# Kernel tuning notes

Hardware: AMD Instinct MI355X
Metric: run time of the kernel (lower is better)

Reference implementation:

```python
import jax, jax.numpy as jnp
import numpy as np

B, T, O, H = 64, 1000, 61, 256
IN0, IN1 = 320, 2 * H  # layer0 input = 8*40 flattened feats; layer1 input = bidirectional concat


def setup_inputs() -> dict:
    key = jax.random.key(0)
    ks = jax.random.split(key, 12)
    rn = lambda k, shape: (jax.random.normal(k, shape, dtype=jnp.float32) * 0.05)
    inp = {}
    inp["batch"] = jax.random.normal(ks[0], (B, T, 8, 40), dtype=jnp.float32)
    lengths = np.random.RandomState(0).randint(T // 2, T + 1, size=B).astype(np.int64)
    inp["lengths"] = jnp.asarray(lengths)
    # GRU params stacked over directions: [2, 3H, in], [2, 3H, H], biases [2, 3H]
    inp["w_ih_l0"] = rn(ks[1], (2, 3 * H, IN0))
    inp["w_hh_l0"] = rn(ks[2], (2, 3 * H, H))
    inp["b_ih_l0"] = rn(ks[3], (2, 3 * H))
    inp["b_hh_l0"] = rn(ks[4], (2, 3 * H))
    inp["w_ih_l1"] = rn(ks[5], (2, 3 * H, IN1))
    inp["w_hh_l1"] = rn(ks[6], (2, 3 * H, H))
    inp["b_ih_l1"] = rn(ks[7], (2, 3 * H))
    inp["b_hh_l1"] = rn(ks[8], (2, 3 * H))
    inp["fc_w"] = rn(ks[9], (O, 2 * H))
    inp["fc_b"] = rn(ks[10], (O,))
    return inp


def _gru_dir(x, w_ih, w_hh, b_ih, b_hh, reverse):
    # x: [T, B, in] -> ys: [T, B, H]; torch GRU cell semantics
    def step(h, xt):
        gi = xt @ w_ih.T + b_ih          # [B, 3H]
        gh = h @ w_hh.T + b_hh           # [B, 3H]
        i_r, i_z, i_n = jnp.split(gi, 3, axis=-1)
        h_r, h_z, h_n = jnp.split(gh, 3, axis=-1)
        r = jax.nn.sigmoid(i_r + h_r)
        z = jax.nn.sigmoid(i_z + h_z)
        n = jnp.tanh(i_n + r * h_n)
        h_new = (1.0 - z) * n + z * h
        return h_new, h_new
    h0 = jnp.zeros((x.shape[1], w_hh.shape[-1]), x.dtype)
    _, ys = jax.lax.scan(step, h0, x, reverse=reverse)
    return ys


def _bigru_layer(x, w_ih, w_hh, b_ih, b_hh):
    fwd = _gru_dir(x, w_ih[0], w_hh[0], b_ih[0], b_hh[0], reverse=False)
    bwd = _gru_dir(x, w_ih[1], w_hh[1], b_ih[1], b_hh[1], reverse=True)
    return jnp.concatenate([fwd, bwd], axis=-1)  # [T, B, 2H]


def reference(batch, lengths, w_ih_l0, w_hh_l0, b_ih_l0, b_hh_l0,
              w_ih_l1, w_hh_l1, b_ih_l1, b_hh_l1, fc_w, fc_b):
    b, t = batch.shape[0], batch.shape[1]
    x = jnp.swapaxes(batch, 2, 3).reshape(b, t, -1)   # transpose(2,3).flatten(2) -> [B,T,320]
    x = jnp.swapaxes(x, 0, 1)                          # [T, B, 320] (time-major like torch GRU)
    h1 = _bigru_layer(x, w_ih_l0, w_hh_l0, b_ih_l0, b_hh_l0)
    h2 = _bigru_layer(h1, w_ih_l1, w_hh_l1, b_ih_l1, b_hh_l1)
    out = h2 @ fc_w.T + fc_b                           # [T, B, O]
    out = jnp.swapaxes(out, 0, 1)                      # [B, T, O]
    # gather first lengths[i] timesteps of each sample, concatenated
    L = np.asarray(lengths)
    mask = np.arange(t)[None, :] < L[:, None]
    bi, ti = np.nonzero(mask)
    return out[bi, ti]                                 # [sum(lengths), O]
```

## Files before the change

kernel.cpp:

```cpp
#include <hip/hip_runtime.h>
#include <cstdint>
#include <cstddef>


typedef __attribute__((ext_vector_type(8))) __bf16 bf16x8;
typedef __attribute__((ext_vector_type(4))) float f32x4;
typedef __attribute__((ext_vector_type(4))) unsigned int u32x4;

#define AS1 __attribute__((address_space(1)))
#define AS3 __attribute__((address_space(3)))

#define LOG2E 1.44269504089f
#define SRZ  (-1.44269504089f)
#define SN   (2.88539008177f)

__device__ __forceinline__ void async_ld16(const void* g, void* l) {
  __builtin_amdgcn_global_load_lds((const AS1 unsigned int*)g,
                                   (AS3 unsigned int*)l, 16, 0, 0);
}

__device__ __forceinline__ f32x4 mfma16(u32x4 a, u32x4 b, f32x4 c) {
  return __builtin_amdgcn_mfma_f32_16x16x32_bf16(
      __builtin_bit_cast(bf16x8, a), __builtin_bit_cast(bf16x8, b), c, 0, 0, 0);
}

__device__ __forceinline__ unsigned short f2b(float f) {
  unsigned int u = __float_as_uint(f);
  u += 0x7fffu + ((u >> 16) & 1u);
  return (unsigned short)(u >> 16);
}
__device__ __forceinline__ float b2f(unsigned short s) {
  return __uint_as_float(((unsigned int)s) << 16);
}
__device__ __forceinline__ float gload(const float* p, size_t i) { return p[i]; }
__device__ __forceinline__ float gload(const unsigned short* p, size_t i) { return b2f(p[i]); }
__device__ __forceinline__ void gstore(float* p, size_t i, float v) { p[i] = v; }
__device__ __forceinline__ void gstore(unsigned short* p, size_t i, float v) { p[i] = f2b(v); }

__device__ __forceinline__ float sigm2(float xs) {
  return __builtin_amdgcn_rcpf(1.0f + __builtin_amdgcn_exp2f(xs));
}
__device__ __forceinline__ float tanh2(float ys) {
  return __builtin_fmaf(-2.0f,
      __builtin_amdgcn_rcpf(1.0f + __builtin_amdgcn_exp2f(ys)), 1.0f);
}

__device__ __forceinline__ void lds_barrier() {
  asm volatile("" ::: "memory");
  __builtin_amdgcn_s_waitcnt(0xC07F);
  __builtin_amdgcn_s_barrier();
  asm volatile("" ::: "memory");
}

__global__ void cast_bf16_kernel(const float* __restrict__ src,
                                 unsigned short* __restrict__ dst, int n) {
  const int i = blockIdx.x * 256 + threadIdx.x;
  if (i < n) dst[i] = f2b(src[i]);
}

__global__ void cast_w_kernel(const float* __restrict__ src,
                              unsigned short* __restrict__ dst, int n,
                              int in_dim) {
  const int i = blockIdx.x * 256 + threadIdx.x;
  if (i < n) {
    const int row = (i / in_dim) % 768;
    const float s = (row < 512) ? SRZ : SN;
    dst[i] = f2b(s * src[i]);
  }
}

__global__ void bias_fuse_kernel(const float* __restrict__ bih,
                                 const float* __restrict__ bhh,
                                 float* __restrict__ fb) {
  const int n = blockIdx.x * 256 + threadIdx.x;
  if (n < 1536) {
    const int dir = n >> 9 >> 1 ? 1 : (n / 768);
    const int rr = n - dir * 768;
    const float s = (rr < 512) ? SRZ : SN;
    float v = bih[dir * 768 + rr];
    if (rr < 512) v += bhh[dir * 768 + rr];
    fb[n] = s * v;
  }
}

__global__ void transpose_x_kernel(const float* __restrict__ batch,
                                   unsigned short* __restrict__ xb) {
  const int t = blockIdx.x, b = blockIdx.y, i = threadIdx.x;
  const float v = batch[((size_t)b * 1000 + t) * 320 + (i & 7) * 40 + (i >> 3)];
  xb[((size_t)t * 64 + b) * 320 + i] = f2b(v);
}

template <typename CT>
__global__ __launch_bounds__(256) void gemm_bt_kernel(
    const unsigned short* __restrict__ A, const unsigned short* __restrict__ W,
    const float* __restrict__ bias, CT* __restrict__ C, int M, int N, int K) {
  __shared__ __align__(16) unsigned short As[4096];
  __shared__ __align__(16) unsigned short Bs[4096];
  const int tid = threadIdx.x;
  const int lane = tid & 63;
  const int wv = tid >> 6;
  const int mBase = blockIdx.x * 128;
  const int nBase = blockIdx.y * 128;

  const int s0 = tid, s1 = tid + 256;
  const int r0 = ((s0 >> 6) << 4) | (s0 & 15), c0 = ((s0 >> 4) & 3) * 8;
  const int r1 = ((s1 >> 6) << 4) | (s1 & 15), c1 = ((s1 >> 4) & 3) * 8;

  const unsigned short* Arow0 = A + (size_t)(mBase + r0) * K + c0;
  const unsigned short* Arow1 = A + (size_t)(mBase + r1) * K + c1;
  const unsigned short* Wrow0 = W + (size_t)(nBase + r0) * K + c0;
  const unsigned short* Wrow1 = W + (size_t)(nBase + r1) * K + c1;

  char* lA = (char*)As;
  char* lB = (char*)Bs;
  char* dstA0 = lA + wv * 1024;
  char* dstA1 = lA + 4096 + wv * 1024;
  char* dstB0 = lB + wv * 1024;
  char* dstB1 = lB + 4096 + wv * 1024;

  f32x4 acc[4][4] = {};
  const int mh = (wv >> 1) * 64, nh = (wv & 1) * 64;
  const u32x4* As4 = (const u32x4*)As;
  const u32x4* Bs4 = (const u32x4*)Bs;

  for (int k0 = 0; k0 < K; k0 += 32) {
    __syncthreads();
    async_ld16(Arow0 + k0, dstA0);
    async_ld16(Arow1 + k0, dstA1);
    async_ld16(Wrow0 + k0, dstB0);
    async_ld16(Wrow1 + k0, dstB1);
    __syncthreads();
    u32x4 a[4], b[4];
#pragma unroll
    for (int mt = 0; mt < 4; ++mt) a[mt] = As4[((mh >> 4) + mt) * 64 + lane];
#pragma unroll
    for (int nt = 0; nt < 4; ++nt) b[nt] = Bs4[((nh >> 4) + nt) * 64 + lane];
#pragma unroll
    for (int mt = 0; mt < 4; ++mt)
#pragma unroll
      for (int nt = 0; nt < 4; ++nt)
        acc[mt][nt] = mfma16(a[mt], b[nt], acc[mt][nt]);
  }
#pragma unroll
  for (int nt = 0; nt < 4; ++nt) {
    const int n = nBase + nh + nt * 16 + (lane & 15);
    const float bn = bias[n];
#pragma unroll
    for (int mt = 0; mt < 4; ++mt) {
      const int mrow = mBase + mh + mt * 16 + ((lane >> 4) << 2);
#pragma unroll
      for (int r = 0; r < 4; ++r)
        gstore(C, (size_t)(mrow + r) * N + n, acc[mt][nt][r] + bn);
    }
  }
}

template <typename GT>
__global__ __launch_bounds__(512, 2) void gru_fast_kernel(
    const GT* __restrict__ gi,
    const unsigned short* __restrict__ whh,
    const float* __restrict__ bhh,
    unsigned short* __restrict__ hout) {
  constexpr int E = (int)sizeof(GT);
  constexpr int CH = (E * 1536) / 1024;
  extern __shared__ __align__(16) char smem[];
  char* wlds = smem;
  char* hl   = smem + 98304;
  char* glds = smem + 98304 + 9216;
  const int tid = threadIdx.x;
  const int lane = tid & 63;
  const int w = tid >> 6;
  const int c = lane & 15;
  const int q = lane >> 4;
  const int dir = blockIdx.x & 1;
  const int sb = (blockIdx.x >> 1) * 16;

  for (int i = tid; i < 4608; i += 512) ((unsigned short*)hl)[i] = 0;

  const int u0 = 32 * w + c;
  const float bhn0 = SN * bhh[dir * 768 + 512 + u0];
  const float bhn1 = SN * bhh[dir * 768 + 512 + u0 + 16];

  const unsigned short* wb =
      whh + (size_t)dir * 196608 + (size_t)u0 * 256 + q * 8;
  u32x4 wv[2][3][6];
#pragma unroll
  for (int j = 0; j < 2; ++j)
#pragma unroll
    for (int g = 0; g < 3; ++g) {
      const unsigned short* p = wb + (size_t)(g * 256 + 16 * j) * 256;
#pragma unroll
      for (int kt = 0; kt < 6; ++kt) wv[j][g][kt] = *(const u32x4*)(p + kt * 32);
#pragma unroll
      for (int kk = 0; kk < 2; ++kk) {
        u32x4 tmp = *(const u32x4*)(p + (6 + kk) * 32);
        *(u32x4*)(wlds + (((w * 12 + (j * 3 + g) * 2 + kk) << 10) + lane * 16)) = tmp;
      }
    }
#pragma unroll
  for (int j = 0; j < 2; ++j)
#pragma unroll
    for (int g = 0; g < 3; ++g)
#pragma unroll
      for (int kt = 0; kt < 6; ++kt)
        asm volatile("" : "+v"(wv[j][g][kt]));

  float h0[4] = {0.f, 0.f, 0.f, 0.f}, h1[4] = {0.f, 0.f, 0.f, 0.f};

  const int t0 = dir ? 999 : 0;
  unsigned short* hp = hout + ((size_t)t0 * 64 + sb) * 512 + dir * 256 + u0;
  const ptrdiff_t gstep = (dir ? -1 : 1) * (ptrdiff_t)(64 * 1536);
  const ptrdiff_t hstep = (dir ? -1 : 1) * (ptrdiff_t)(64 * 512);

  char* gdw = glds + w * (1536 * E);
  const int off0 = (c ^ ((q & 1) << 4)) * E;
  const int off1 = ((c + 16) ^ ((q & 1) << 4)) * E;
  const char* grb0 = gdw + (q * 4) * (96 * E) + off0;
  const char* grb1 = gdw + (q * 4) * (96 * E) + off1;
  const GT* gs[CH];
#pragma unroll
  for (int i = 0; i < CH; ++i) {
    const int p    = i * 64 + lane;
    const int s    = p / (6 * E);
    const int rem  = p - s * (6 * E);
    const int g    = rem / (2 * E);
    const int subp = rem - g * (2 * E);
    const int sub  = subp ^ (((s >> 2) & 1) * E);
    const int col  = sub * (16 / E);
    gs[i] = gi + ((size_t)t0 * 64 + sb + s) * 1536 + dir * 768 + 32 * w +
            g * 256 + col;
  }
#pragma unroll
  for (int i = 0; i < CH; ++i) {
    async_ld16(gs[i], gdw + i * 1024);
    gs[i] += gstep;
  }

  __syncthreads();

  const char* habase = hl + c * 576 + q * 16;
  const int hw0 = q * 4 * 288 + u0;

  for (int step = 0; step < 1000; ++step) {
    u32x4 a[8];
#pragma unroll
    for (int kt = 0; kt < 8; ++kt) a[kt] = *(const u32x4*)(habase + kt * 64);
    lds_barrier();

    f32x4 acc[2][3] = {};
#pragma unroll
    for (int kt = 0; kt < 6; ++kt)
#pragma unroll
      for (int j = 0; j < 2; ++j)
#pragma unroll
        for (int g = 0; g < 3; ++g)
          acc[j][g] = mfma16(a[kt], wv[j][g][kt], acc[j][g]);
#pragma unroll
    for (int kk = 0; kk < 2; ++kk) {
      u32x4 bf[2][3];
#pragma unroll
      for (int j = 0; j < 2; ++j)
#pragma unroll
        for (int g = 0; g < 3; ++g)
          bf[j][g] = *(const u32x4*)(
              wlds + (((w * 12 + (j * 3 + g) * 2 + kk) << 10) + lane * 16));
#pragma unroll
      for (int j = 0; j < 2; ++j)
#pragma unroll
        for (int g = 0; g < 3; ++g)
          acc[j][g] = mfma16(a[6 + kk], bf[j][g], acc[j][g]);
    }

    asm volatile("s_waitcnt vmcnt(0)" ::: "memory");
    float pv0[3][4], pv1[3][4];
#pragma unroll
    for (int r = 0; r < 4; ++r)
#pragma unroll
      for (int g = 0; g < 3; ++g) {
        pv0[g][r] = gload((const GT*)(grb0 + (r * 96 + g * 32) * E), (size_t)0);
        pv1[g][r] = gload((const GT*)(grb1 + (r * 96 + g * 32) * E), (size_t)0);
      }

    unsigned short* hls = (unsigned short*)hl;
#pragma unroll
    for (int r = 0; r < 4; ++r) {
      const float rr0 = sigm2(pv0[0][r] + acc[0][0][r]);
      const float zz0 = sigm2(pv0[1][r] + acc[0][1][r]);
      const float nn0 = tanh2(__builtin_fmaf(rr0, acc[0][2][r] + bhn0, pv0[2][r]));
      const float hv0 = __builtin_fmaf(zz0, h0[r] - nn0, nn0);
      h0[r] = hv0;
      const float rr1 = sigm2(pv1[0][r] + acc[1][0][r]);
      const float zz1 = sigm2(pv1[1][r] + acc[1][1][r]);
      const float nn1 = tanh2(__builtin_fmaf(rr1, acc[1][2][r] + bhn1, pv1[2][r]));
      const float hv1 = __builtin_fmaf(zz1, h1[r] - nn1, nn1);
      h1[r] = hv1;
      const unsigned short hb0 = f2b(hv0), hb1 = f2b(hv1);
      hls[hw0 + r * 288] = hb0;
      hls[hw0 + r * 288 + 16] = hb1;
      hp[(size_t)(q * 4 + r) * 512] = hb0;
      hp[(size_t)(q * 4 + r) * 512 + 16] = hb1;
    }

#pragma unroll
    for (int i = 0; i < CH; ++i) {
      async_ld16(gs[i], gdw + i * 1024);
      gs[i] += gstep;
    }
    hp += hstep;
    lds_barrier();
  }
}

template <typename GT>
__global__ __launch_bounds__(1024) void gru_layer_kernel(
    const GT* __restrict__ gi, const unsigned short* __restrict__ whh,
    const float* __restrict__ bhh, unsigned short* __restrict__ hout) {
  __shared__ __align__(16) unsigned short hbf[16][264];
  __shared__ __align__(16) float gh[16][780];
  const int tid = threadIdx.x;
  const int lane = tid & 63;
  const int wv = tid >> 6;
  const int dir = blockIdx.x & 1;
  const int sb = (blockIdx.x >> 1) * 16;
  const int j = tid & 255;
  const int si = tid >> 8;

  float hreg[4] = {0.f, 0.f, 0.f, 0.f};
#pragma unroll
  for (int i = 0; i < 4; ++i) hbf[si + i * 4][j] = 0;

  const float bh_n = SN * bhh[dir * 768 + 512 + j];

  const unsigned short* wl = whh + (size_t)dir * 768 * 256 +
                             (size_t)(wv * 48 + (lane & 15)) * 256 +
                             ((lane >> 4) * 8);
  const char* habase = (const char*)hbf + (lane & 15) * 528 + ((lane >> 4) << 4);
  const int srow = (lane >> 4) * 4;

  __syncthreads();

  for (int step = 0; step < 1000; ++step) {
    const int t = dir ? (999 - step) : step;
    float p_ir[4], p_iz[4], p_in[4];
#pragma unroll
    for (int i = 0; i < 4; ++i) {
      const int s = si + i * 4;
      const size_t gib = ((size_t)t * 64 + (sb + s)) * 1536 + dir * 768 + j;
      p_ir[i] = gload(gi, gib);
      p_iz[i] = gload(gi, gib + 256);
      p_in[i] = gload(gi, gib + 512);
    }
    u32x4 a[8];
#pragma unroll
    for (int kt = 0; kt < 8; ++kt) a[kt] = *(const u32x4*)(habase + kt * 64);
#pragma unroll
    for (int ntd = 0; ntd < 3; ++ntd) {
      f32x4 acc = {0.f, 0.f, 0.f, 0.f};
#pragma unroll
      for (int kt = 0; kt < 8; ++kt) {
        u32x4 bfrag = *(const u32x4*)(wl + ntd * (16 * 256) + kt * 32);
        acc = mfma16(a[kt], bfrag, acc);
      }
      const int gcol = (wv * 3 + ntd) * 16 + (lane & 15);
#pragma unroll
      for (int r = 0; r < 4; ++r) gh[srow + r][gcol] = acc[r];
    }
    __syncthreads();
#pragma unroll
    for (int i = 0; i < 4; ++i) {
      const int s = si + i * 4;
      const float r = sigm2(p_ir[i] + gh[s][j]);
      const float z = sigm2(p_iz[i] + gh[s][256 + j]);
      const float n = tanh2(__builtin_fmaf(r, gh[s][512 + j] + bh_n, p_in[i]));
      const float h = __builtin_fmaf(z, hreg[i] - n, n);
      hreg[i] = h;
      const unsigned short hb = f2b(h);
      hbf[s][j] = hb;
      hout[((size_t)t * 64 + (sb + s)) * 512 + dir * 256 + j] = hb;
    }
    __syncthreads();
  }
}

__global__ void prefix_kernel(const int* __restrict__ raw,
                              int* __restrict__ pref, int* __restrict__ lens) {
  if (threadIdx.x == 0) {
    const int stride = (raw[1] == 0 && raw[3] == 0 && raw[5] == 0) ? 2 : 1;
    int a = 0;
    for (int b = 0; b < 64; ++b) {
      const int L = raw[b * stride];
      pref[b] = a;
      lens[b] = L;
      a += L;
    }
  }
}

__global__ __launch_bounds__(256) void fc_kernel(
    const unsigned short* __restrict__ h2, const unsigned short* __restrict__ fcw,
    const float* __restrict__ fcb, const int* __restrict__ lens,
    const int* __restrict__ pref, float* __restrict__ out) {
  __shared__ __align__(16) unsigned short hrow[4][512];
  const int b = blockIdx.y;
  const int sub = threadIdx.x >> 6, lane = threadIdx.x & 63;
  const int t = blockIdx.x * 4 + sub;
  *(u32x4*)&hrow[sub][lane * 8] =
      *(const u32x4*)&h2[((size_t)t * 64 + b) * 512 + lane * 8];
  __syncthreads();
  const int len = lens[b];
  if (lane < 61 && t < len) {
    float acc = fcb[lane];
    const unsigned short* wr = fcw + (size_t)lane * 512;
#pragma unroll 4
    for (int k = 0; k < 512; k += 8) {
      u32x4 w4 = *(const u32x4*)(wr + k);
      u32x4 h4 = *(const u32x4*)(&hrow[sub][k]);
#pragma unroll
      for (int qq = 0; qq < 4; ++qq) {
        acc += __uint_as_float(w4[qq] << 16) * __uint_as_float(h4[qq] << 16);
        acc += __uint_as_float(w4[qq] & 0xffff0000u) * __uint_as_float(h4[qq] & 0xffff0000u);
      }
    }
    out[((size_t)pref[b] + t) * 61 + lane] = acc;
  }
}

template <typename GT>
static void run_pipeline(const float* batch, const int* lengths_raw,
                         const float* w_ih_l0, const float* w_hh_l0,
                         const float* b_ih_l0, const float* b_hh_l0,
                         const float* w_ih_l1, const float* w_hh_l1,
                         const float* b_ih_l1, const float* b_hh_l1,
                         const float* fc_w, const float* fc_b, float* out,
                         char* ws, hipStream_t stream) {
  size_t off = 0;
  auto alloc = [&](size_t bytes) -> char* {
    char* p = ws + off;
    off += (bytes + 255) & ~(size_t)255;
    return p;
  };
  char* pool = alloc((size_t)64000 * 512 * 2);
  unsigned short* xb = (unsigned short*)pool;
  unsigned short* h1 = (unsigned short*)pool;
  unsigned short* h2 = (unsigned short*)pool;
  GT*             gi   = (GT*)alloc((size_t)64064 * 1536 * sizeof(GT));
  unsigned short* wih0 = (unsigned short*)alloc((size_t)1536 * 320 * 2);
  unsigned short* wih1 = (unsigned short*)alloc((size_t)1536 * 512 * 2);
  unsigned short* whh0 = (unsigned short*)alloc((size_t)1536 * 256 * 2);
  unsigned short* whh1 = (unsigned short*)alloc((size_t)1536 * 256 * 2);
  unsigned short* fcwb = (unsigned short*)alloc((size_t)61 * 512 * 2);
  float*          fb0  = (float*)alloc(1536 * 4);
  float*          fb1  = (float*)alloc(1536 * 4);
  int*            pref = (int*)alloc(256);
  int*            lens = (int*)alloc(256);

  auto castw = [&](const float* s, unsigned short* d, int n, int in_dim) {
    cast_w_kernel<<<dim3((n + 255) / 256), dim3(256), 0, stream>>>(s, d, n, in_dim);
  };
  castw(w_ih_l0, wih0, 2 * 768 * 320, 320);
  castw(w_hh_l0, whh0, 2 * 768 * 256, 256);
  castw(w_ih_l1, wih1, 2 * 768 * 512, 512);
  castw(w_hh_l1, whh1, 2 * 768 * 256, 256);
  cast_bf16_kernel<<<dim3((61 * 512 + 255) / 256), dim3(256), 0, stream>>>(
      fc_w, fcwb, 61 * 512);
  bias_fuse_kernel<<<dim3(6), dim3(256), 0, stream>>>(b_ih_l0, b_hh_l0, fb0);
  bias_fuse_kernel<<<dim3(6), dim3(256), 0, stream>>>(b_ih_l1, b_hh_l1, fb1);

  transpose_x_kernel<<<dim3(1000, 64), dim3(320), 0, stream>>>(batch, xb);

  const int GRU_LDS = 98304 + 9216 + 8 * 1536 * (int)sizeof(GT);
  const bool big_lds =
      hipFuncSetAttribute(reinterpret_cast<const void*>(gru_fast_kernel<GT>),
                          hipFuncAttributeMaxDynamicSharedMemorySize,
                          GRU_LDS) == hipSuccess;

  auto gru = [&](GT* g, unsigned short* w, const float* b, unsigned short* h) {
    if (big_lds)
      gru_fast_kernel<GT><<<dim3(8), dim3(512), GRU_LDS, stream>>>(g, w, b, h);
    else
      gru_layer_kernel<GT><<<dim3(8), dim3(1024), 0, stream>>>(g, w, b, h);
  };

  gemm_bt_kernel<GT><<<dim3(500, 12), dim3(256), 0, stream>>>(
      xb, wih0, fb0, gi, 64000, 1536, 320);
  gru(gi, whh0, b_hh_l0, h1);
  gemm_bt_kernel<GT><<<dim3(500, 12), dim3(256), 0, stream>>>(
      h1, wih1, fb1, gi, 64000, 1536, 512);
  gru(gi, whh1, b_hh_l1, h2);

  prefix_kernel<<<dim3(1), dim3(64), 0, stream>>>(lengths_raw, pref, lens);
  fc_kernel<<<dim3(250, 64), dim3(256), 0, stream>>>(h2, fcwb, fc_b, lens, pref, out);
}

extern "C" void kernel_launch(void* const* d_in, const int* in_sizes, int n_in,
                              void* d_out, int out_size, void* d_ws, size_t ws_size,
                              hipStream_t stream) {
  (void)in_sizes; (void)n_in; (void)out_size;
  const float* batch   = (const float*)d_in[0];
  const int*   lengths = (const int*)d_in[1];
  const float* w_ih_l0 = (const float*)d_in[2];
  const float* w_hh_l0 = (const float*)d_in[3];
  const float* b_ih_l0 = (const float*)d_in[4];
  const float* b_hh_l0 = (const float*)d_in[5];
  const float* w_ih_l1 = (const float*)d_in[6];
  const float* w_hh_l1 = (const float*)d_in[7];
  const float* b_ih_l1 = (const float*)d_in[8];
  const float* b_hh_l1 = (const float*)d_in[9];
  const float* fc_w    = (const float*)d_in[10];
  const float* fc_b    = (const float*)d_in[11];
  float* out = (float*)d_out;
  char* ws = (char*)d_ws;

  const size_t NEED_FP32 = 470000000ull;
  if (ws_size >= NEED_FP32) {
    run_pipeline<float>(batch, lengths, w_ih_l0, w_hh_l0, b_ih_l0, b_hh_l0,
                        w_ih_l1, w_hh_l1, b_ih_l1, b_hh_l1, fc_w, fc_b, out,
                        ws, stream);
  } else {
    run_pipeline<unsigned short>(batch, lengths, w_ih_l0, w_hh_l0, b_ih_l0,
                                 b_hh_l0, w_ih_l1, w_hh_l1, b_ih_l1, b_hh_l1,
                                 fc_w, fc_b, out, ws, stream);
  }
}
```

Measured before the change: 4.536 ms.

## Double-buffer GRU hidden state and interleave gate MFMAs with activations

For the bf16 gate-input path, the hidden-state LDS buffer is double-buffered so each step reads one copy and writes the other. This removes the barrier that sat between the h read and the matmul. The recurrent matmul is split per gate (r, then n, then z) so the sigmoid and tanh work on earlier gates can overlap the MFMAs of later ones. The async prefetch of the next step's gate inputs is issued earlier in the step. The cost is extra LDS per block and more live registers, and it relies on a single end-of-step barrier being enough for correctness.

```diff
diff --git a/kernel.cpp b/kernel.cpp
--- a/kernel.cpp
+++ b/kernel.cpp
@@ -155,6 +155,22 @@
   }
 }
 
+#define GBLOCK(G)                                                              \
+  {                                                                            \
+    _Pragma("unroll") for (int kt = 0; kt < 6; ++kt) {                         \
+      acc[0][G] = mfma16(a[kt], wv[0][G][kt], acc[0][G]);                      \
+      acc[1][G] = mfma16(a[kt], wv[1][G][kt], acc[1][G]);                      \
+    }                                                                          \
+    _Pragma("unroll") for (int kk = 0; kk < 2; ++kk) {                         \
+      u32x4 bf0 = *(const u32x4*)(wlds +                                       \
+          (((w * 12 + (0 * 3 + (G)) * 2 + kk) << 10) + lane * 16));            \
+      u32x4 bf1 = *(const u32x4*)(wlds +                                       \
+          (((w * 12 + (1 * 3 + (G)) * 2 + kk) << 10) + lane * 16));            \
+      acc[0][G] = mfma16(a[6 + kk], bf0, acc[0][G]);                           \
+      acc[1][G] = mfma16(a[6 + kk], bf1, acc[1][G]);                           \
+    }                                                                          \
+  }
+
 template <typename GT>
 __global__ __launch_bounds__(512, 2) void gru_fast_kernel(
     const GT* __restrict__ gi,
@@ -163,10 +179,12 @@
     unsigned short* __restrict__ hout) {
   constexpr int E = (int)sizeof(GT);
   constexpr int CH = (E * 1536) / 1024;
+  constexpr bool DB = (E == 2);
+  constexpr int HB = DB ? 18432 : 9216;
   extern __shared__ __align__(16) char smem[];
   char* wlds = smem;
   char* hl   = smem + 98304;
-  char* glds = smem + 98304 + 9216;
+  char* glds = smem + 98304 + HB;
   const int tid = threadIdx.x;
   const int lane = tid & 63;
   const int w = tid >> 6;
@@ -175,7 +193,7 @@
   const int dir = blockIdx.x & 1;
   const int sb = (blockIdx.x >> 1) * 16;
 
-  for (int i = tid; i < 4608; i += 512) ((unsigned short*)hl)[i] = 0;
+  for (int i = tid; i < HB / 2; i += 512) ((unsigned short*)hl)[i] = 0;
 
   const int u0 = 32 * w + c;
   const float bhn0 = SN * bhh[dir * 768 + 512 + u0];
@@ -241,35 +259,15 @@
   const char* habase = hl + c * 576 + q * 16;
   const int hw0 = q * 4 * 288 + u0;
 
-  for (int step = 0; step < 1000; ++step) {
+  auto body = [&](int rd, int wr) {
     u32x4 a[8];
 #pragma unroll
-    for (int kt = 0; kt < 8; ++kt) a[kt] = *(const u32x4*)(habase + kt * 64);
-    lds_barrier();
+    for (int kt = 0; kt < 8; ++kt)
+      a[kt] = *(const u32x4*)(habase + rd + kt * 64);
+    if constexpr (!DB) lds_barrier();
 
     f32x4 acc[2][3] = {};
-#pragma unroll
-    for (int kt = 0; kt < 6; ++kt)
-#pragma unroll
-      for (int j = 0; j < 2; ++j)
-#pragma unroll
-        for (int g = 0; g < 3; ++g)
-          acc[j][g] = mfma16(a[kt], wv[j][g][kt], acc[j][g]);
-#pragma unroll
-    for (int kk = 0; kk < 2; ++kk) {
-      u32x4 bf[2][3];
-#pragma unroll
-      for (int j = 0; j < 2; ++j)
-#pragma unroll
-        for (int g = 0; g < 3; ++g)
-          bf[j][g] = *(const u32x4*)(
-              wlds + (((w * 12 + (j * 3 + g) * 2 + kk) << 10) + lane * 16));
-#pragma unroll
-      for (int j = 0; j < 2; ++j)
-#pragma unroll
-        for (int g = 0; g < 3; ++g)
-          acc[j][g] = mfma16(a[6 + kk], bf[j][g], acc[j][g]);
-    }
+    GBLOCK(0)
 
     asm volatile("s_waitcnt vmcnt(0)" ::: "memory");
     float pv0[3][4], pv1[3][4];
@@ -280,19 +278,39 @@
         pv0[g][r] = gload((const GT*)(grb0 + (r * 96 + g * 32) * E), (size_t)0);
         pv1[g][r] = gload((const GT*)(grb1 + (r * 96 + g * 32) * E), (size_t)0);
       }
-
-    unsigned short* hls = (unsigned short*)hl;
+    asm volatile("s_waitcnt lgkmcnt(0)" ::: "memory");
+#pragma unroll
+    for (int i = 0; i < CH; ++i) {
+      async_ld16(gs[i], gdw + i * 1024);
+      gs[i] += gstep;
+    }
+
+    float rr0[4], rr1[4];
 #pragma unroll
     for (int r = 0; r < 4; ++r) {
-      const float rr0 = sigm2(pv0[0][r] + acc[0][0][r]);
+      rr0[r] = sigm2(pv0[0][r] + acc[0][0][r]);
+      rr1[r] = sigm2(pv1[0][r] + acc[1][0][r]);
+    }
+
+    GBLOCK(2)
+
+    float nn0[4], nn1[4];
+#pragma unroll
+    for (int r = 0; r < 4; ++r) {
+      nn0[r] = tanh2(__builtin_fmaf(rr0[r], acc[0][2][r] + bhn0, pv0[2][r]));
+      nn1[r] = tanh2(__builtin_fmaf(rr1[r], acc[1][2][r] + bhn1, pv1[2][r]));
+    }
+
+    GBLOCK(1)
+
+    unsigned short* hls = (unsigned short*)(hl + wr);
+#pragma unroll
+    for (int r = 0; r < 4; ++r) {
       const float zz0 = sigm2(pv0[1][r] + acc[0][1][r]);
-      const float nn0 = tanh2(__builtin_fmaf(rr0, acc[0][2][r] + bhn0, pv0[2][r]));
-      const float hv0 = __builtin_fmaf(zz0, h0[r] - nn0, nn0);
+      const float hv0 = __builtin_fmaf(zz0, h0[r] - nn0[r], nn0[r]);
       h0[r] = hv0;
-      const float rr1 = sigm2(pv1[0][r] + acc[1][0][r]);
       const float zz1 = sigm2(pv1[1][r] + acc[1][1][r]);
-      const float nn1 = tanh2(__builtin_fmaf(rr1, acc[1][2][r] + bhn1, pv1[2][r]));
-      const float hv1 = __builtin_fmaf(zz1, h1[r] - nn1, nn1);
+      const float hv1 = __builtin_fmaf(zz1, h1[r] - nn1[r], nn1[r]);
       h1[r] = hv1;
       const unsigned short hb0 = f2b(hv0), hb1 = f2b(hv1);
       hls[hw0 + r * 288] = hb0;
@@ -300,15 +318,19 @@
       hp[(size_t)(q * 4 + r) * 512] = hb0;
       hp[(size_t)(q * 4 + r) * 512 + 16] = hb1;
     }
-
-#pragma unroll
-    for (int i = 0; i < CH; ++i) {
-      async_ld16(gs[i], gdw + i * 1024);
-      gs[i] += gstep;
-    }
     hp += hstep;
     lds_barrier();
-  }
+  };
+
+  if constexpr (DB) {
+    for (int it = 0; it < 500; ++it) {
+      body(0, 9216);
+      body(9216, 0);
+    }
+  } else {
+    for (int step = 0; step < 1000; ++step) body(0, 0);
+  }
+  asm volatile("s_waitcnt vmcnt(0)" ::: "memory");
 }
 
 template <typename GT>
@@ -468,7 +490,8 @@
 
   transpose_x_kernel<<<dim3(1000, 64), dim3(320), 0, stream>>>(batch, xb);
 
-  const int GRU_LDS = 98304 + 9216 + 8 * 1536 * (int)sizeof(GT);
+  const int HB = (sizeof(GT) == 2) ? 18432 : 9216;
+  const int GRU_LDS = 98304 + HB + 8 * 1536 * (int)sizeof(GT);
   const bool big_lds =
       hipFuncSetAttribute(reinterpret_cast<const void*>(gru_fast_kernel<GT>),
                           hipFuncAttributeMaxDynamicSharedMemorySize,
```

Measured after the change: 4.196 ms. -7.5%, faster.
